# Kernel tuning notes

Hardware: AMD Instinct MI355X
Metric: run time of the kernel (lower is better)

Reference implementation:

```python
import jax, jax.numpy as jnp
import numpy as np

CHUNK = 128  # single steady-state chunk tier (T divisible by 128)
DECAY_MIN = 0.005


def setup_inputs() -> dict:
    key = jax.random.key(0)
    k0, k1, k2, k3, k4 = jax.random.split(key, 5)
    B, H, T, K = 4, 16, 2048, 64
    r = jax.random.normal(k0, (B, H, T, K), jnp.float32) * 0.5
    k = jax.random.normal(k1, (B, H, T, K), jnp.float32) * 0.5
    v = jax.random.normal(k2, (B, H, T, K), jnp.float32)
    # log-space decay (negative); mild magnitude keeps exp() of cumulative
    # in-chunk decays within fp32 range (torch original upcasts to fp64)
    w = -(jax.random.uniform(k3, (B, H, T, K), jnp.float32) * 0.2 + 0.01)
    u = jax.random.normal(k4, (1, H, 1, K), jnp.float32) * 0.5
    wkv_state = jnp.zeros((B, H, K, K), jnp.float32)
    return {"r": r, "k": k, "v": v, "w": w, "u": u, "wkv_state": wkv_state}


def _chunked_wkv(r, k, v, w, u, wkv_state):
    B, H, T, K = r.shape
    Tc = CHUNK
    N = T // Tc
    # decay preprocessing (log space)
    w_decay = jnp.clip(jnp.exp(w), DECAY_MIN, None)
    w_log = jnp.log(w_decay)
    wc = w_log.reshape(B, H, N, Tc, K)
    wc_cum = jnp.cumsum(wc, axis=-2)                       # inclusive cumsum
    shifted = jnp.pad(wc_cum[..., :-1, :], ((0, 0), (0, 0), (0, 0), (1, 0), (0, 0)))
    ws = wc.sum(axis=-2, keepdims=True)                    # (B,H,N,1,K)
    w_inter = jnp.exp(ws - wc_cum)                          # (B,H,N,Tc,K)
    w_intra = jnp.exp(wc_cum - wc)
    ws_e = jnp.exp(jnp.swapaxes(ws, -1, -2))               # (B,H,N,K,1)

    rc = r.reshape(B, H, N, Tc, K)
    kc = k.reshape(B, H, N, Tc, K)
    vc = v.reshape(B, H, N, Tc, K)

    # numerically-centered intra-chunk decays (offset at chunk midpoint)
    off = shifted[..., Tc // 2:Tc // 2 + 1, :]
    r_dec = jnp.exp(shifted - off)
    k_inv = jnp.exp(off - wc_cum)

    # intra-chunk attention: strictly-lower-triangular + u-bonus diagonal
    a = jnp.einsum('bhnik,bhnjk->bhnij', rc * r_dec, kc * k_inv)
    a = jnp.tril(a, -1)
    diag = jnp.einsum('bhntk,bhntk->bhnt', rc, u[:, :, None] * kc)
    a = a + diag[..., :, None] * jnp.eye(Tc, dtype=a.dtype)
    out = jnp.einsum('bhnij,bhnjv->bhniv', a, vc)

    # inter-chunk: sequential state carry via scan
    wkv = jnp.einsum('bhntk,bhntv->bhnkv', kc * w_inter, vc)   # (B,H,N,K,K)

    def step(state, inp):
        ws_i, wkv_i = inp
        return state * ws_i + wkv_i, state

    ws_s = jnp.moveaxis(ws_e, 2, 0)    # (N,B,H,K,1)
    wkv_s = jnp.moveaxis(wkv, 2, 0)    # (N,B,H,K,K)
    final_state, states = jax.lax.scan(step, wkv_state, (ws_s, wkv_s))
    states = jnp.moveaxis(states, 0, 2)  # (B,H,N,K,K) — state entering chunk n

    out = out + jnp.einsum('bhntk,bhnkv->bhntv', rc * w_intra, states)
    return out.reshape(B, H, T, K), final_state


def reference(r, k, v, w, u, wkv_state):
    return _chunked_wkv(r, k, v, w, u, wkv_state)
```

## Files before the change

### kernel.cpp

```cpp
#include <hip/hip_runtime.h>

#define TC 128
#define KD 64
#define WLOG_MIN (-5.2983174f)

typedef __attribute__((ext_vector_type(8))) short short8;
typedef __attribute__((ext_vector_type(4))) short short4_t;
typedef __attribute__((ext_vector_type(4))) float f32x4;

__device__ __forceinline__ unsigned short f2bf(float x) {
  union { float f; unsigned int u; } c; c.f = x;
  unsigned int u = c.u + 0x7fffu + ((c.u >> 16) & 1u);
  return (unsigned short)(u >> 16);
}
__device__ __forceinline__ float bf2f(unsigned short x) {
  union { unsigned int u; float f; } c; c.u = ((unsigned int)x) << 16; return c.f;
}


__global__ __launch_bounds__(256, 2)
void rwkv_intra_mfma(const float* __restrict__ rr, const float* __restrict__ kk_,
                     const float* __restrict__ vv, const float* __restrict__ ww,
                     const float* __restrict__ uu, float* __restrict__ out,
                     unsigned short* __restrict__ wkv_u16, float* __restrict__ wse_ws,
                     unsigned short* __restrict__ rw_u16, int H, int N) {
  __shared__ alignas(16) unsigned short rd_s[TC * KD];
  __shared__ alignas(16) unsigned short ki_s[TC * KD];
  __shared__ alignas(16) unsigned short kiT_s[KD * TC];
  __shared__ alignas(16) unsigned short vT_s[KD * TC];
  __shared__ alignas(16) unsigned short Ast[4][16 * 40];
  __shared__ float diag[TC];
  __shared__ float segtot[4][KD];
  __shared__ float wsoffs[KD];

  const int bid = blockIdx.x;
  const int n = bid % N, bh = bid / N, h = bh % H;
  const size_t base = ((size_t)bh * N + n) * (TC * KD);
  const float *rg = rr + base, *kg = kk_ + base, *vg = vv + base, *wg = ww + base;

  const int tid = threadIdx.x;
  const int lk = tid & 63;
  const int wv = tid >> 6;

  float wl[32];
  {
    float c = 0.f;
    #pragma unroll
    for (int tt = 0; tt < 32; ++tt) {
      wl[tt] = fmaxf(wg[(wv * 32 + tt) * KD + lk], WLOG_MIN);
      c += wl[tt];
    }
    segtot[wv][lk] = c;
  }
  __syncthreads();
  const float s0 = segtot[0][lk], s1 = segtot[1][lk], s2 = segtot[2][lk], s3 = segtot[3][lk];
  const float myoff = s0 + s1;
  const float segofs = (wv == 0) ? 0.f : (wv == 1) ? s0 : (wv == 2) ? (s0 + s1) : (s0 + s1 + s2);
  if (wv == 0) {
    const float wsum = s0 + s1 + s2 + s3;
    wsoffs[lk] = __expf(wsum - myoff);
    wse_ws[((size_t)bh * N + n) * KD + lk] = __expf(wsum);
  }
  const float eoff = __expf(myoff);

  {
    float c = segofs;
    const float uk = uu[h * KD + lk];
    unsigned short* rwg = rw_u16 + base;
    short8 kib8, vb8;
    #pragma unroll
    for (int tt = 0; tt < 32; ++tt) {
      const int t = wv * 32 + tt;
      float rv = rg[t * KD + lk], kv = kg[t * KD + lk], vvv = vg[t * KD + lk];
      const int nat = t * KD + ((((lk >> 3) ^ (t & 7)) << 3) | (lk & 7));
      float e1 = __expf(c - myoff);
      rd_s[nat] = f2bf(rv * e1);
      rwg[t * KD + lk] = f2bf(rv * e1 * eoff);
      unsigned short kib = f2bf(kv * __expf(myoff - c - wl[tt]));
      ki_s[nat] = kib;
      kib8[tt & 7] = (short)kib;
      vb8[tt & 7] = (short)f2bf(vvv);
      float d = rv * uk * kv;
      #pragma unroll
      for (int o = 32; o > 0; o >>= 1) d += __shfl_xor(d, o, 64);
      if (lk == 0) diag[t] = d;
      c += wl[tt];
      if ((tt & 7) == 7) {
        const int g = t >> 3;
        *(short8*)&kiT_s[lk * TC + ((g ^ (lk & 7)) << 3)] = kib8;
        *(short8*)&vT_s [lk * TC + ((g ^ (lk & 7)) << 3)] = vb8;
      }
    }
  }
  __syncthreads();

  const int lane = tid & 63, quad = lane >> 4, l16 = lane & 15;

  {
    f32x4 acc[4] = {{0,0,0,0},{0,0,0,0},{0,0,0,0},{0,0,0,0}};
    const int kd = wv * 16 + l16;
    #pragma unroll
    for (int ks = 0; ks < 4; ++ks) {
      const int g = ks * 4 + quad;
      short8 a = *(const short8*)&kiT_s[kd * TC + ((g ^ (kd & 7)) << 3)];
      #pragma unroll
      for (int nn = 0; nn < 4; ++nn) {
        const int vd = nn * 16 + l16;
        short8 b = *(const short8*)&vT_s[vd * TC + ((g ^ (vd & 7)) << 3)];
        acc[nn] = __builtin_amdgcn_mfma_f32_16x16x32_bf16(a, b, acc[nn], 0, 0, 0);
      }
    }
    unsigned short* wkvg = wkv_u16 + ((size_t)bh * N + n) * (KD * KD);
    #pragma unroll
    for (int nn = 0; nn < 4; ++nn)
      #pragma unroll
      for (int reg = 0; reg < 4; ++reg) {
        const int kde = wv * 16 + quad * 4 + reg;
        wkvg[kde * KD + nn * 16 + l16] = f2bf(acc[nn][reg] * wsoffs[kde]);
      }
  }

  #pragma unroll
  for (int half = 0; half < 2; ++half) {
    const int ib = half ? (7 - wv) : wv;
    const int i0 = ib * 16;
    const int irow = i0 + l16;
    short8 b0 = *(const short8*)&rd_s[irow * KD + ((quad ^ (irow & 7)) << 3)];
    short8 b1 = *(const short8*)&rd_s[irow * KD + (((4 + quad) ^ (irow & 7)) << 3)];
    const float diag_i = diag[irow];
    f32x4 oacc[4] = {{0,0,0,0},{0,0,0,0},{0,0,0,0},{0,0,0,0}};
    const int npairs = (ib + 2) >> 1;
    unsigned short* astw = &Ast[wv][0];
    for (int jp = 0; jp < npairs; ++jp) {
      #pragma unroll
      for (int jj = 0; jj < 2; ++jj) {
        const int j = jp * 2 + jj;
        short4_t pk;
        if (j <= ib) {
          const int jrow = j * 16 + l16;
          short8 a0 = *(const short8*)&ki_s[jrow * KD + ((quad ^ (jrow & 7)) << 3)];
          short8 a1 = *(const short8*)&ki_s[jrow * KD + (((4 + quad) ^ (jrow & 7)) << 3)];
          f32x4 at = {0, 0, 0, 0};
          at = __builtin_amdgcn_mfma_f32_16x16x32_bf16(a0, b0, at, 0, 0, 0);
          at = __builtin_amdgcn_mfma_f32_16x16x32_bf16(a1, b1, at, 0, 0, 0);
          #pragma unroll
          for (int reg = 0; reg < 4; ++reg) {
            const int je = j * 16 + quad * 4 + reg;
            float val = at[reg];
            if (j == ib) val = (je < irow) ? val : ((je == irow) ? diag_i : 0.f);
            pk[reg] = (short)f2bf(val);
          }
        } else {
          pk = (short4_t)0;
        }
        *(short4_t*)&astw[l16 * 40 + jj * 16 + quad * 4] = pk;
      }
      short8 af = *(const short8*)&astw[l16 * 40 + quad * 8];
      #pragma unroll
      for (int nn = 0; nn < 4; ++nn) {
        const int vd = nn * 16 + l16;
        const int g = jp * 4 + quad;
        short8 bv = *(const short8*)&vT_s[vd * TC + ((g ^ (vd & 7)) << 3)];
        oacc[nn] = __builtin_amdgcn_mfma_f32_16x16x32_bf16(af, bv, oacc[nn], 0, 0, 0);
      }
    }
    float* og = out + base;
    #pragma unroll
    for (int nn = 0; nn < 4; ++nn)
      #pragma unroll
      for (int reg = 0; reg < 4; ++reg) {
        const int ie = i0 + quad * 4 + reg;
        og[ie * KD + nn * 16 + l16] = oacc[nn][reg];
      }
  }
}

__global__ __launch_bounds__(256)
void rwkv_scan_kernel(const unsigned short* __restrict__ wkv_u16,
                      const float* __restrict__ wse_ws,
                      const float* __restrict__ st_in,
                      unsigned short* __restrict__ statesT_u16,
                      float* __restrict__ final_out, int N) {
  const int bh = blockIdx.x >> 2;
  const int vq = blockIdx.x & 3;
  const int tid = threadIdx.x;
  const size_t sbase = (size_t)bh * (KD * KD);
  float stt[4];
  int kd[4], vd[4], swz[4];
  #pragma unroll
  for (int i = 0; i < 4; ++i) {
    int e = tid + i * 256;
    kd[i] = e >> 4; vd[i] = vq * 16 + (e & 15);
    swz[i] = vd[i] * KD + ((((kd[i] >> 3) ^ (vd[i] & 7)) << 3) | (kd[i] & 7));
    stt[i] = st_in[sbase + kd[i] * KD + vd[i]];
  }
  float nwk[4], nwe[4];
  #pragma unroll
  for (int i = 0; i < 4; ++i) {
    nwk[i] = bf2f(wkv_u16[(size_t)bh * N * (KD * KD) + kd[i] * KD + vd[i]]);
    nwe[i] = wse_ws[(size_t)bh * N * KD + kd[i]];
  }
  for (int nn = 0; nn < N; ++nn) {
    float cwk[4], cwe[4];
    #pragma unroll
    for (int i = 0; i < 4; ++i) { cwk[i] = nwk[i]; cwe[i] = nwe[i]; }
    if (nn + 1 < N) {
      const size_t b2 = (size_t)bh * N + nn + 1;
      #pragma unroll
      for (int i = 0; i < 4; ++i) {
        nwk[i] = bf2f(wkv_u16[b2 * (KD * KD) + kd[i] * KD + vd[i]]);
        nwe[i] = wse_ws[b2 * KD + kd[i]];
      }
    }
    unsigned short* so = statesT_u16 + ((size_t)bh * N + nn) * (KD * KD);
    #pragma unroll
    for (int i = 0; i < 4; ++i) {
      so[swz[i]] = f2bf(stt[i]);
      stt[i] = stt[i] * cwe[i] + cwk[i];
    }
  }
  #pragma unroll
  for (int i = 0; i < 4; ++i)
    final_out[sbase + kd[i] * KD + vd[i]] = stt[i];
}

__global__ __launch_bounds__(256)
void rwkv_inter_mfma(const unsigned short* __restrict__ rw_u16,
                     const unsigned short* __restrict__ statesT_u16,
                     float* __restrict__ out, int N) {
  __shared__ alignas(16) unsigned short rw_s[TC * KD];
  __shared__ alignas(16) unsigned short stT_s[KD * KD];
  const int bid = blockIdx.x;
  const int n = bid % N, bh = bid / N;
  const size_t base = ((size_t)bh * N + n) * (TC * KD);
  const int tid = threadIdx.x;
  {
    const short8* rwg = (const short8*)(rw_u16 + base);
    #pragma unroll
    for (int x = 0; x < 4; ++x) {
      int m = tid + x * 256;
      int t = m >> 3, g = m & 7;
      *(short8*)&rw_s[t * KD + ((g ^ (t & 7)) << 3)] = rwg[m];
    }
    const short8* sg = (const short8*)(statesT_u16 + ((size_t)bh * N + n) * (KD * KD));
    #pragma unroll
    for (int x = 0; x < 2; ++x) {
      int m = tid + x * 256;
      *(short8*)&stT_s[m * 8] = sg[m];
    }
  }
  __syncthreads();
  const int lane = tid & 63, quad = lane >> 4, l16 = lane & 15, wv = tid >> 6;
  #pragma unroll
  for (int half = 0; half < 2; ++half) {
    const int ib = wv + half * 4;
    const int i0 = ib * 16, irow = i0 + l16;
    short8 a0 = *(const short8*)&rw_s[irow * KD + ((quad ^ (irow & 7)) << 3)];
    short8 a1 = *(const short8*)&rw_s[irow * KD + (((4 + quad) ^ (irow & 7)) << 3)];
    f32x4 acc[4] = {{0,0,0,0},{0,0,0,0},{0,0,0,0},{0,0,0,0}};
    #pragma unroll
    for (int nn = 0; nn < 4; ++nn) {
      const int vd = nn * 16 + l16;
      short8 bb0 = *(const short8*)&stT_s[vd * KD + ((quad ^ (vd & 7)) << 3)];
      short8 bb1 = *(const short8*)&stT_s[vd * KD + (((4 + quad) ^ (vd & 7)) << 3)];
      acc[nn] = __builtin_amdgcn_mfma_f32_16x16x32_bf16(a0, bb0, acc[nn], 0, 0, 0);
      acc[nn] = __builtin_amdgcn_mfma_f32_16x16x32_bf16(a1, bb1, acc[nn], 0, 0, 0);
    }
    float* og = out + base;
    #pragma unroll
    for (int nn = 0; nn < 4; ++nn)
      #pragma unroll
      for (int reg = 0; reg < 4; ++reg) {
        const int ie = i0 + quad * 4 + reg;
        og[ie * KD + nn * 16 + l16] += acc[nn][reg];
      }
  }
}

extern "C" void kernel_launch(void* const* d_in, const int* in_sizes, int n_in,
                              void* d_out, int out_size, void* d_ws, size_t ws_size,
                              hipStream_t stream) {
  const float* r = (const float*)d_in[0];
  const float* k = (const float*)d_in[1];
  const float* v = (const float*)d_in[2];
  const float* w = (const float*)d_in[3];
  const float* u = (const float*)d_in[4];
  const float* st0 = (const float*)d_in[5];
  float* out = (float*)d_out;

  const int BH = in_sizes[5] / (KD * KD);
  const int H = in_sizes[4] / KD;
  const int T = in_sizes[0] / (BH * KD);
  const int N = T / TC;

  unsigned short* wkv_u16 = (unsigned short*)d_ws;
  float* wse_ws = (float*)(wkv_u16 + (size_t)BH * N * KD * KD);
  unsigned short* statesT_u16 = (unsigned short*)(wse_ws + (size_t)BH * N * KD);
  unsigned short* rw_u16 = statesT_u16 + (size_t)BH * N * KD * KD;
  float* final_out = out + (size_t)in_sizes[0];

  rwkv_intra_mfma<<<BH * N, 256, 0, stream>>>(r, k, v, w, u, out, wkv_u16, wse_ws, rw_u16, H, N);
  rwkv_scan_kernel<<<BH * 4, 256, 0, stream>>>(wkv_u16, wse_ws, st0, statesT_u16, final_out, N);
  rwkv_inter_mfma<<<BH * N, 256, 0, stream>>>(rw_u16, statesT_u16, out, N);
}
```

Before: 220.8 us.

## Fuse state scan with inter-chunk output and shrink intra kernel LDS

The sequential state scan and the inter-chunk output matmul are merged into one kernel. Each scan block keeps the running state in LDS and applies it to that chunk's rw rows right away, so the statesT buffer and its global round trip are gone. The intra kernel drops the transposed k buffer and reads k transposed out of the swizzled ki_s with scalar gathers. It also packs diag into global bf16 and aliases segtot with Ast, cutting LDS enough to allow 3 blocks per CU. The cost is that the fused kernel runs only BH*4 = 256 blocks through a serial loop over chunks, and the inter matmul loses the wide parallelism it had as its own launch.

```diff
diff --git a/kernel.cpp b/kernel.cpp
--- a/kernel.cpp
+++ b/kernel.cpp
@@ -18,25 +18,25 @@
 }
 
 
-__global__ __launch_bounds__(256, 2)
+__global__ __launch_bounds__(256, 3)
 void rwkv_intra_mfma(const float* __restrict__ rr, const float* __restrict__ kk_,
                      const float* __restrict__ vv, const float* __restrict__ ww,
                      const float* __restrict__ uu, float* __restrict__ out,
                      unsigned short* __restrict__ wkv_u16, float* __restrict__ wse_ws,
-                     unsigned short* __restrict__ rw_u16, int H, int N) {
+                     unsigned short* __restrict__ rw_u16, unsigned short* __restrict__ diag_u16,
+                     int H, int N) {
   __shared__ alignas(16) unsigned short rd_s[TC * KD];
   __shared__ alignas(16) unsigned short ki_s[TC * KD];
-  __shared__ alignas(16) unsigned short kiT_s[KD * TC];
   __shared__ alignas(16) unsigned short vT_s[KD * TC];
-  __shared__ alignas(16) unsigned short Ast[4][16 * 40];
-  __shared__ float diag[TC];
-  __shared__ float segtot[4][KD];
-  __shared__ float wsoffs[KD];
+  __shared__ alignas(16) unsigned char su_raw[5120];
+  float* segtot = (float*)su_raw;
+  unsigned short* Ast = (unsigned short*)su_raw;
 
   const int bid = blockIdx.x;
   const int n = bid % N, bh = bid / N, h = bh % H;
   const size_t base = ((size_t)bh * N + n) * (TC * KD);
   const float *rg = rr + base, *kg = kk_ + base, *vg = vv + base, *wg = ww + base;
+  unsigned short* diagg = diag_u16 + (size_t)bid * TC;
 
   const int tid = threadIdx.x;
   const int lk = tid & 63;
@@ -50,45 +50,50 @@
       wl[tt] = fmaxf(wg[(wv * 32 + tt) * KD + lk], WLOG_MIN);
       c += wl[tt];
     }
-    segtot[wv][lk] = c;
+    segtot[wv * 64 + lk] = c;
   }
   __syncthreads();
-  const float s0 = segtot[0][lk], s1 = segtot[1][lk], s2 = segtot[2][lk], s3 = segtot[3][lk];
+  const float s0 = segtot[0 * 64 + lk], s1 = segtot[1 * 64 + lk];
+  const float s2 = segtot[2 * 64 + lk], s3 = segtot[3 * 64 + lk];
   const float myoff = s0 + s1;
   const float segofs = (wv == 0) ? 0.f : (wv == 1) ? s0 : (wv == 2) ? (s0 + s1) : (s0 + s1 + s2);
-  if (wv == 0) {
-    const float wsum = s0 + s1 + s2 + s3;
-    wsoffs[lk] = __expf(wsum - myoff);
-    wse_ws[((size_t)bh * N + n) * KD + lk] = __expf(wsum);
-  }
+  const float wsum = s0 + s1 + s2 + s3;
+  const float wsoff_own = __expf(wsum - myoff);
+  if (wv == 0) wse_ws[((size_t)bh * N + n) * KD + lk] = __expf(wsum);
   const float eoff = __expf(myoff);
 
   {
     float c = segofs;
     const float uk = uu[h * KD + lk];
     unsigned short* rwg = rw_u16 + base;
-    short8 kib8, vb8;
+    short8 vb8;
+    float darr[8];
     #pragma unroll
     for (int tt = 0; tt < 32; ++tt) {
       const int t = wv * 32 + tt;
       float rv = rg[t * KD + lk], kv = kg[t * KD + lk], vvv = vg[t * KD + lk];
-      const int nat = t * KD + ((((lk >> 3) ^ (t & 7)) << 3) | (lk & 7));
+      const int slot = (lk >> 3) ^ (t & 7) ^ ((t >> 3) & 7);
+      const int nat = t * KD + (slot << 3) + (lk & 7);
       float e1 = __expf(c - myoff);
       rd_s[nat] = f2bf(rv * e1);
       rwg[t * KD + lk] = f2bf(rv * e1 * eoff);
-      unsigned short kib = f2bf(kv * __expf(myoff - c - wl[tt]));
-      ki_s[nat] = kib;
-      kib8[tt & 7] = (short)kib;
+      ki_s[nat] = f2bf(kv * __expf(myoff - c - wl[tt]));
       vb8[tt & 7] = (short)f2bf(vvv);
-      float d = rv * uk * kv;
-      #pragma unroll
-      for (int o = 32; o > 0; o >>= 1) d += __shfl_xor(d, o, 64);
-      if (lk == 0) diag[t] = d;
+      darr[tt & 7] = rv * uk * kv;
       c += wl[tt];
       if ((tt & 7) == 7) {
         const int g = t >> 3;
-        *(short8*)&kiT_s[lk * TC + ((g ^ (lk & 7)) << 3)] = kib8;
-        *(short8*)&vT_s [lk * TC + ((g ^ (lk & 7)) << 3)] = vb8;
+        *(short8*)&vT_s[lk * TC + ((g ^ (lk & 7)) << 3)] = vb8;
+        #pragma unroll
+        for (int o = 32; o > 0; o >>= 1)
+          #pragma unroll
+          for (int q = 0; q < 8; ++q) darr[q] += __shfl_xor(darr[q], o, 64);
+        if (lk == 0) {
+          short8 dpk;
+          #pragma unroll
+          for (int q = 0; q < 8; ++q) dpk[q] = (short)f2bf(darr[q]);
+          *(short8*)&diagg[g * 8] = dpk;
+        }
       }
     }
   }
@@ -98,26 +103,31 @@
 
   {
     f32x4 acc[4] = {{0,0,0,0},{0,0,0,0},{0,0,0,0},{0,0,0,0}};
-    const int kd = wv * 16 + l16;
+    const int kdg = wv * 2 + (l16 >> 3), kd7 = l16 & 7;
     #pragma unroll
     for (int ks = 0; ks < 4; ++ks) {
-      const int g = ks * 4 + quad;
-      short8 a = *(const short8*)&kiT_s[kd * TC + ((g ^ (kd & 7)) << 3)];
+      short8 a;
+      #pragma unroll
+      for (int j = 0; j < 8; ++j) {
+        const int t = ks * 32 + quad * 8 + j;
+        a[j] = (short)ki_s[t * KD + (((kdg ^ (t & 7) ^ ((t >> 3) & 7)) << 3) + kd7)];
+      }
       #pragma unroll
       for (int nn = 0; nn < 4; ++nn) {
         const int vd = nn * 16 + l16;
-        short8 b = *(const short8*)&vT_s[vd * TC + ((g ^ (vd & 7)) << 3)];
+        short8 b = *(const short8*)&vT_s[vd * TC + (((ks * 4 + quad) ^ (vd & 7)) << 3)];
         acc[nn] = __builtin_amdgcn_mfma_f32_16x16x32_bf16(a, b, acc[nn], 0, 0, 0);
       }
     }
+    float wso[4];
+    #pragma unroll
+    for (int reg = 0; reg < 4; ++reg) wso[reg] = __shfl(wsoff_own, wv * 16 + quad * 4 + reg, 64);
     unsigned short* wkvg = wkv_u16 + ((size_t)bh * N + n) * (KD * KD);
     #pragma unroll
     for (int nn = 0; nn < 4; ++nn)
       #pragma unroll
-      for (int reg = 0; reg < 4; ++reg) {
-        const int kde = wv * 16 + quad * 4 + reg;
-        wkvg[kde * KD + nn * 16 + l16] = f2bf(acc[nn][reg] * wsoffs[kde]);
-      }
+      for (int reg = 0; reg < 4; ++reg)
+        wkvg[(wv * 16 + quad * 4 + reg) * KD + nn * 16 + l16] = f2bf(acc[nn][reg] * wso[reg]);
   }
 
   #pragma unroll
@@ -125,12 +135,13 @@
     const int ib = half ? (7 - wv) : wv;
     const int i0 = ib * 16;
     const int irow = i0 + l16;
-    short8 b0 = *(const short8*)&rd_s[irow * KD + ((quad ^ (irow & 7)) << 3)];
-    short8 b1 = *(const short8*)&rd_s[irow * KD + (((4 + quad) ^ (irow & 7)) << 3)];
-    const float diag_i = diag[irow];
+    const int rsw = (irow & 7) ^ ((irow >> 3) & 7);
+    short8 b0 = *(const short8*)&rd_s[irow * KD + ((quad ^ rsw) << 3)];
+    short8 b1 = *(const short8*)&rd_s[irow * KD + (((4 + quad) ^ rsw) << 3)];
+    const float diag_i = bf2f(diagg[irow]);
     f32x4 oacc[4] = {{0,0,0,0},{0,0,0,0},{0,0,0,0},{0,0,0,0}};
     const int npairs = (ib + 2) >> 1;
-    unsigned short* astw = &Ast[wv][0];
+    unsigned short* astw = Ast + wv * 640;
     for (int jp = 0; jp < npairs; ++jp) {
       #pragma unroll
       for (int jj = 0; jj < 2; ++jj) {
@@ -138,8 +149,9 @@
         short4_t pk;
         if (j <= ib) {
           const int jrow = j * 16 + l16;
-          short8 a0 = *(const short8*)&ki_s[jrow * KD + ((quad ^ (jrow & 7)) << 3)];
-          short8 a1 = *(const short8*)&ki_s[jrow * KD + (((4 + quad) ^ (jrow & 7)) << 3)];
+          const int jsw = (jrow & 7) ^ ((jrow >> 3) & 7);
+          short8 a0 = *(const short8*)&ki_s[jrow * KD + ((quad ^ jsw) << 3)];
+          short8 a1 = *(const short8*)&ki_s[jrow * KD + (((4 + quad) ^ jsw) << 3)];
           f32x4 at = {0, 0, 0, 0};
           at = __builtin_amdgcn_mfma_f32_16x16x32_bf16(a0, b0, at, 0, 0, 0);
           at = __builtin_amdgcn_mfma_f32_16x16x32_bf16(a1, b1, at, 0, 0, 0);
@@ -159,8 +171,7 @@
       #pragma unroll
       for (int nn = 0; nn < 4; ++nn) {
         const int vd = nn * 16 + l16;
-        const int g = jp * 4 + quad;
-        short8 bv = *(const short8*)&vT_s[vd * TC + ((g ^ (vd & 7)) << 3)];
+        short8 bv = *(const short8*)&vT_s[vd * TC + (((jp * 4 + quad) ^ (vd & 7)) << 3)];
         oacc[nn] = __builtin_amdgcn_mfma_f32_16x16x32_bf16(af, bv, oacc[nn], 0, 0, 0);
       }
     }
@@ -168,113 +179,83 @@
     #pragma unroll
     for (int nn = 0; nn < 4; ++nn)
       #pragma unroll
+      for (int reg = 0; reg < 4; ++reg)
+        og[(i0 + quad * 4 + reg) * KD + nn * 16 + l16] = oacc[nn][reg];
+  }
+}
+
+__global__ __launch_bounds__(256)
+void rwkv_scan_inter(const unsigned short* __restrict__ wkv_u16,
+                     const float* __restrict__ wse_ws,
+                     const float* __restrict__ st_in,
+                     const unsigned short* __restrict__ rw_u16,
+                     float* __restrict__ out, float* __restrict__ final_out, int N) {
+  __shared__ alignas(16) unsigned short sT[16 * KD];
+  const int bh = blockIdx.x >> 2, vq = blockIdx.x & 3;
+  const int tid = threadIdx.x;
+  const int vd_l = tid & 15;
+  const int kd0 = (tid >> 4) * 4;
+  const size_t sbase = (size_t)bh * (KD * KD);
+
+  float stt[4];
+  #pragma unroll
+  for (int j = 0; j < 4; ++j) stt[j] = st_in[sbase + (kd0 + j) * KD + vq * 16 + vd_l];
+
+  float nwk[4], nwe[4];
+  #pragma unroll
+  for (int j = 0; j < 4; ++j) {
+    nwk[j] = bf2f(wkv_u16[(size_t)bh * N * (KD * KD) + (kd0 + j) * KD + vq * 16 + vd_l]);
+    nwe[j] = wse_ws[(size_t)bh * N * KD + kd0 + j];
+  }
+
+  const int lane = tid & 63, wv = tid >> 6, quad = lane >> 4, l16 = lane & 15;
+  for (int n = 0; n < N; ++n) {
+    #pragma unroll
+    for (int j = 0; j < 4; ++j) {
+      const int kd = kd0 + j;
+      sT[vd_l * KD + ((((kd >> 3) ^ (vd_l & 7)) << 3) | (kd & 7))] = f2bf(stt[j]);
+    }
+    __syncthreads();
+
+    float cwk[4], cwe[4];
+    #pragma unroll
+    for (int j = 0; j < 4; ++j) { cwk[j] = nwk[j]; cwe[j] = nwe[j]; }
+    if (n + 1 < N) {
+      const size_t b2 = (size_t)bh * N + n + 1;
+      #pragma unroll
+      for (int j = 0; j < 4; ++j) {
+        nwk[j] = bf2f(wkv_u16[b2 * (KD * KD) + (kd0 + j) * KD + vq * 16 + vd_l]);
+        nwe[j] = wse_ws[b2 * KD + kd0 + j];
+      }
+    }
+
+    const unsigned short* rwg = rw_u16 + ((size_t)bh * N + n) * (TC * KD);
+    float* og = out + ((size_t)bh * N + n) * (TC * KD);
+    #pragma unroll
+    for (int half = 0; half < 2; ++half) {
+      const int mt = wv + half * 4;
+      const int trow = mt * 16 + l16;
+      short8 a0 = *(const short8*)&rwg[trow * KD + quad * 8];
+      short8 a1 = *(const short8*)&rwg[trow * KD + 32 + quad * 8];
+      short8 b0 = *(const short8*)&sT[l16 * KD + ((quad ^ (l16 & 7)) << 3)];
+      short8 b1 = *(const short8*)&sT[l16 * KD + (((4 + quad) ^ (l16 & 7)) << 3)];
+      f32x4 acc = {0, 0, 0, 0};
+      acc = __builtin_amdgcn_mfma_f32_16x16x32_bf16(a0, b0, acc, 0, 0, 0);
+      acc = __builtin_amdgcn_mfma_f32_16x16x32_bf16(a1, b1, acc, 0, 0, 0);
+      #pragma unroll
       for (int reg = 0; reg < 4; ++reg) {
-        const int ie = i0 + quad * 4 + reg;
-        og[ie * KD + nn * 16 + l16] = oacc[nn][reg];
-      }
-  }
-}
-
-__global__ __launch_bounds__(256)
-void rwkv_scan_kernel(const unsigned short* __restrict__ wkv_u16,
-                      const float* __restrict__ wse_ws,
-                      const float* __restrict__ st_in,
-                      unsigned short* __restrict__ statesT_u16,
-                      float* __restrict__ final_out, int N) {
-  const int bh = blockIdx.x >> 2;
-  const int vq = blockIdx.x & 3;
-  const int tid = threadIdx.x;
-  const size_t sbase = (size_t)bh * (KD * KD);
-  float stt[4];
-  int kd[4], vd[4], swz[4];
-  #pragma unroll
-  for (int i = 0; i < 4; ++i) {
-    int e = tid + i * 256;
-    kd[i] = e >> 4; vd[i] = vq * 16 + (e & 15);
-    swz[i] = vd[i] * KD + ((((kd[i] >> 3) ^ (vd[i] & 7)) << 3) | (kd[i] & 7));
-    stt[i] = st_in[sbase + kd[i] * KD + vd[i]];
-  }
-  float nwk[4], nwe[4];
-  #pragma unroll
-  for (int i = 0; i < 4; ++i) {
-    nwk[i] = bf2f(wkv_u16[(size_t)bh * N * (KD * KD) + kd[i] * KD + vd[i]]);
-    nwe[i] = wse_ws[(size_t)bh * N * KD + kd[i]];
-  }
-  for (int nn = 0; nn < N; ++nn) {
-    float cwk[4], cwe[4];
-    #pragma unroll
-    for (int i = 0; i < 4; ++i) { cwk[i] = nwk[i]; cwe[i] = nwe[i]; }
-    if (nn + 1 < N) {
-      const size_t b2 = (size_t)bh * N + nn + 1;
-      #pragma unroll
-      for (int i = 0; i < 4; ++i) {
-        nwk[i] = bf2f(wkv_u16[b2 * (KD * KD) + kd[i] * KD + vd[i]]);
-        nwe[i] = wse_ws[b2 * KD + kd[i]];
-      }
-    }
-    unsigned short* so = statesT_u16 + ((size_t)bh * N + nn) * (KD * KD);
-    #pragma unroll
-    for (int i = 0; i < 4; ++i) {
-      so[swz[i]] = f2bf(stt[i]);
-      stt[i] = stt[i] * cwe[i] + cwk[i];
-    }
-  }
-  #pragma unroll
-  for (int i = 0; i < 4; ++i)
-    final_out[sbase + kd[i] * KD + vd[i]] = stt[i];
-}
-
-__global__ __launch_bounds__(256)
-void rwkv_inter_mfma(const unsigned short* __restrict__ rw_u16,
-                     const unsigned short* __restrict__ statesT_u16,
-                     float* __restrict__ out, int N) {
-  __shared__ alignas(16) unsigned short rw_s[TC * KD];
-  __shared__ alignas(16) unsigned short stT_s[KD * KD];
-  const int bid = blockIdx.x;
-  const int n = bid % N, bh = bid / N;
-  const size_t base = ((size_t)bh * N + n) * (TC * KD);
-  const int tid = threadIdx.x;
-  {
-    const short8* rwg = (const short8*)(rw_u16 + base);
-    #pragma unroll
-    for (int x = 0; x < 4; ++x) {
-      int m = tid + x * 256;
-      int t = m >> 3, g = m & 7;
-      *(short8*)&rw_s[t * KD + ((g ^ (t & 7)) << 3)] = rwg[m];
-    }
-    const short8* sg = (const short8*)(statesT_u16 + ((size_t)bh * N + n) * (KD * KD));
-    #pragma unroll
-    for (int x = 0; x < 2; ++x) {
-      int m = tid + x * 256;
-      *(short8*)&stT_s[m * 8] = sg[m];
-    }
-  }
-  __syncthreads();
-  const int lane = tid & 63, quad = lane >> 4, l16 = lane & 15, wv = tid >> 6;
-  #pragma unroll
-  for (int half = 0; half < 2; ++half) {
-    const int ib = wv + half * 4;
-    const int i0 = ib * 16, irow = i0 + l16;
-    short8 a0 = *(const short8*)&rw_s[irow * KD + ((quad ^ (irow & 7)) << 3)];
-    short8 a1 = *(const short8*)&rw_s[irow * KD + (((4 + quad) ^ (irow & 7)) << 3)];
-    f32x4 acc[4] = {{0,0,0,0},{0,0,0,0},{0,0,0,0},{0,0,0,0}};
-    #pragma unroll
-    for (int nn = 0; nn < 4; ++nn) {
-      const int vd = nn * 16 + l16;
-      short8 bb0 = *(const short8*)&stT_s[vd * KD + ((quad ^ (vd & 7)) << 3)];
-      short8 bb1 = *(const short8*)&stT_s[vd * KD + (((4 + quad) ^ (vd & 7)) << 3)];
-      acc[nn] = __builtin_amdgcn_mfma_f32_16x16x32_bf16(a0, bb0, acc[nn], 0, 0, 0);
-      acc[nn] = __builtin_amdgcn_mfma_f32_16x16x32_bf16(a1, bb1, acc[nn], 0, 0, 0);
-    }
-    float* og = out + base;
-    #pragma unroll
-    for (int nn = 0; nn < 4; ++nn)
-      #pragma unroll
-      for (int reg = 0; reg < 4; ++reg) {
-        const int ie = i0 + quad * 4 + reg;
-        og[ie * KD + nn * 16 + l16] += acc[nn][reg];
-      }
-  }
+        const size_t oi = (size_t)(mt * 16 + quad * 4 + reg) * KD + vq * 16 + l16;
+        og[oi] += acc[reg];
+      }
+    }
+
+    #pragma unroll
+    for (int j = 0; j < 4; ++j) stt[j] = stt[j] * cwe[j] + cwk[j];
+    __syncthreads();
+  }
+  #pragma unroll
+  for (int j = 0; j < 4; ++j)
+    final_out[sbase + (kd0 + j) * KD + vq * 16 + vd_l] = stt[j];
 }
 
 extern "C" void kernel_launch(void* const* d_in, const int* in_sizes, int n_in,
@@ -295,11 +276,12 @@
 
   unsigned short* wkv_u16 = (unsigned short*)d_ws;
   float* wse_ws = (float*)(wkv_u16 + (size_t)BH * N * KD * KD);
-  unsigned short* statesT_u16 = (unsigned short*)(wse_ws + (size_t)BH * N * KD);
-  unsigned short* rw_u16 = statesT_u16 + (size_t)BH * N * KD * KD;
+  unsigned short* rw_u16 = (unsigned short*)(wse_ws + (size_t)BH * N * KD);
+  unsigned short* diag_u16 = rw_u16 + (size_t)BH * T * KD;
   float* final_out = out + (size_t)in_sizes[0];
 
-  rwkv_intra_mfma<<<BH * N, 256, 0, stream>>>(r, k, v, w, u, out, wkv_u16, wse_ws, rw_u16, H, N);
-  rwkv_scan_kernel<<<BH * 4, 256, 0, stream>>>(wkv_u16, wse_ws, st0, statesT_u16, final_out, N);
-  rwkv_inter_mfma<<<BH * N, 256, 0, stream>>>(rw_u16, statesT_u16, out, N);
-}
+  rwkv_intra_mfma<<<BH * N, 256, 0, stream>>>(r, k, v, w, u, out, wkv_u16, wse_ws,
+                                              rw_u16, diag_u16, H, N);
+  rwkv_scan_inter<<<BH * 4, 256, 0, stream>>>(wkv_u16, wse_ws, st0, rw_u16,
+                                              out, final_out, N);
+}
```

New measurement: 205.2 us. 1.08x faster.
